# Kernel tuning notes

Hardware: AMD Instinct MI355X
Metric: run time of the kernel (lower is better)

The kernel has to match this reference:

```python
import jax, jax.numpy as jnp
import numpy as np

# Brevitas-style per-tensor affine (symmetric) quantization:
#   scale = max|x| / qmax  (stats-derived, treated as constant)
#   q     = clamp(round(x/scale), qmin, qmax) * scale

def _quant_pt(x, bits):
    qmax = 2.0 ** (bits - 1) - 1.0
    qmin = -(2.0 ** (bits - 1))
    scale = jax.lax.stop_gradient(jnp.max(jnp.abs(x))) / qmax
    scale = jnp.maximum(scale, jnp.asarray(1e-8, x.dtype))
    q = jnp.clip(jnp.round(x / scale), qmin, qmax)
    return q * scale, scale


def setup_inputs() -> dict:
    key = jax.random.key(0)
    k1, k2, k3 = jax.random.split(key, 3)
    in_features, out_features, tokens = 4096, 4096, 8192
    inp = jax.random.normal(k1, (tokens, in_features), dtype=jnp.float32)
    # Kaiming-ish init for linear weight [out, in]
    W = jax.random.normal(k2, (out_features, in_features), dtype=jnp.float32) / np.sqrt(in_features)
    b = jax.random.normal(k3, (out_features,), dtype=jnp.float32) * 0.01
    return {"inp": inp, "W": W, "b": b}


def reference(inp, W, b):
    # input quant: Int8 act per-tensor (QuantIdentity default)
    x_dq, s_in = _quant_pt(inp, 8)
    # weight quant: 4-bit per-tensor
    w_dq, s_w = _quant_pt(W, 4)
    # bias quant: Int32 with scale = s_in * s_w
    s_b = s_in * s_w
    b_dq = jnp.round(b / s_b) * s_b  # int32 range never clips realistic biases
    # matmul in dequantized domain (numerically equal to int GEMM * s_in*s_w)
    y = jnp.einsum('ti,oi->to', x_dq, w_dq) + b_dq
    # output quant: Int8 act per-tensor
    y_dq, _ = _quant_pt(y, 8)
    return y_dq
```

## Files before the change

### kernel.cpp

```cpp
#include <hip/hip_runtime.h>


typedef int v4i __attribute__((ext_vector_type(4)));
typedef int v16i __attribute__((ext_vector_type(16)));

#define AS1(p) ((const __attribute__((address_space(1))) void*)(p))
#define AS3(p) ((__attribute__((address_space(3))) void*)(p))

#define GM 8192
#define GN 4096
#define GK 4096
#define NBN 16
#define NWG 512
#define CH 1088
#define HT 17408

__global__ __launch_bounds__(256) void maxabs2_kernel(const float* __restrict__ x, int n4x,
                                                      unsigned* __restrict__ slotx,
                                                      const float* __restrict__ w, int n4w,
                                                      unsigned* __restrict__ slotw) {
  __shared__ float red[4];
  const float4* src;
  unsigned* slot;
  int n4, bid, nb;
  if (blockIdx.x < 1024) { src = (const float4*)x; slot = slotx; n4 = n4x; bid = blockIdx.x; nb = 1024; }
  else                   { src = (const float4*)w; slot = slotw; n4 = n4w; bid = blockIdx.x - 1024; nb = 512; }
  int tid = bid * 256 + threadIdx.x;
  int stride = nb * 256;
  float m = 0.0f;
  for (int i = tid; i < n4; i += stride) {
    float4 v = src[i];
    m = fmaxf(m, fmaxf(fmaxf(fabsf(v.x), fabsf(v.y)), fmaxf(fabsf(v.z), fabsf(v.w))));
  }
  for (int off = 32; off; off >>= 1) m = fmaxf(m, __shfl_xor(m, off));
  if ((threadIdx.x & 63) == 0) red[threadIdx.x >> 6] = m;
  __syncthreads();
  if (threadIdx.x == 0)
    atomicMax(slot, __float_as_uint(fmaxf(fmaxf(red[0], red[1]), fmaxf(red[2], red[3]))));
}

__global__ __launch_bounds__(256) void quant2_kernel(const float* __restrict__ x,
                                                     signed char* __restrict__ qx, int n4x,
                                                     const unsigned* __restrict__ slotx,
                                                     const float* __restrict__ w,
                                                     signed char* __restrict__ qw, int n4w,
                                                     const unsigned* __restrict__ slotw) {
  const float4* src;
  int* dst;
  int n4, bid, nb;
  float qmaxv, qlo, qhi;
  const unsigned* slot;
  if (blockIdx.x < 1024) {
    src = (const float4*)x; dst = (int*)qx; n4 = n4x; bid = blockIdx.x; nb = 1024;
    slot = slotx; qmaxv = 127.0f; qlo = -128.0f; qhi = 127.0f;
  } else {
    src = (const float4*)w; dst = (int*)qw; n4 = n4w; bid = blockIdx.x - 1024; nb = 512;
    slot = slotw; qmaxv = 7.0f; qlo = -8.0f; qhi = 7.0f;
  }
  float s = fmaxf(__uint_as_float(*slot) / qmaxv, 1e-8f);
  float inv = 1.0f / s;
  int tid = bid * 256 + threadIdx.x;
  int stride = nb * 256;
  for (int i = tid; i < n4; i += stride) {
    float4 v = src[i];
    int a0 = (int)fminf(fmaxf(rintf(v.x * inv), qlo), qhi);
    int a1 = (int)fminf(fmaxf(rintf(v.y * inv), qlo), qhi);
    int a2 = (int)fminf(fmaxf(rintf(v.z * inv), qlo), qhi);
    int a3 = (int)fminf(fmaxf(rintf(v.w * inv), qlo), qhi);
    dst[i] = (a0 & 255) | ((a1 & 255) << 8) | ((a2 & 255) << 16) | ((a3 & 255) << 24);
  }
}

template <bool BF16OUT>
__global__ __launch_bounds__(512, 2) void gemm_i8_kernel(const signed char* __restrict__ Xq,
                                                         const signed char* __restrict__ Wq,
                                                         const float* __restrict__ bias,
                                                         const unsigned* __restrict__ slots,
                                                         void* __restrict__ Yout,
                                                         unsigned* __restrict__ maxY) {
  __shared__ signed char smem[8 * HT];
  const int tid = threadIdx.x;
  const int wid = tid >> 6, lane = tid & 63;
  const int wr = wid >> 2, wc = wid & 3;
  const int l31 = lane & 31, lg2 = lane >> 5;

  const int bid = (int)blockIdx.x;
  const int swz = (bid & 7) * (NWG / 8) + (bid >> 3);
  const int brow = (swz / NBN) * 256;
  const int bcol = (swz % NBN) * 256;

  const int srr = tid >> 3;
  const int sgl = (tid & 7) ^ (srr & 7);

  int aoff[4], asw[4], boff[2], bsw[2];
#pragma unroll
  for (int mm = 0; mm < 4; ++mm) {
    int hr = wr * 64 + (mm & 1) * 32 + l31;
    aoff[mm] = (hr >> 3) * CH + (hr & 7) * 128;
    asw[mm] = hr & 7;
  }
#pragma unroll
  for (int nn = 0; nn < 2; ++nn) {
    int hr = wc * 32 + l31;
    boff[nn] = (hr >> 3) * CH + (hr & 7) * 128;
    bsw[nn] = hr & 7;
  }

#define ASLOT(db, h) (smem + ((db) * 2 + (h)) * HT)
#define BSLOT(db, h) (smem + 4 * HT + ((db) * 2 + (h)) * HT)
#define STAGE(gptr, grow0, kofs, slot)                                                        \
  {                                                                                           \
    const signed char* _s0 = (gptr) + (size_t)((grow0) + srr) * GK + (kofs) + sgl * 16;       \
    __builtin_amdgcn_global_load_lds(AS1(_s0), AS3((slot) + wid * CH), 16, 0, 0);             \
    __builtin_amdgcn_global_load_lds(AS1(_s0 + (size_t)64 * GK),                              \
                                     AS3((slot) + (8 + wid) * CH), 16, 0, 0);                 \
  }
#define LDA32(mm, db, ks) \
  *(const v4i*)(ASLOT(db, (mm) >> 1) + aoff[mm] + ((((ks)*2 + lg2) ^ asw[mm]) << 4))
#define LDB32(nn, db, ks) \
  *(const v4i*)(BSLOT(db, nn) + boff[nn] + ((((ks)*2 + lg2) ^ bsw[nn]) << 4))
#define MFMA8(AF, BF)                                                                         \
  __builtin_amdgcn_s_setprio(1);                                                              \
  _Pragma("unroll") for (int mm = 0; mm < 4; ++mm)                                            \
      _Pragma("unroll") for (int nn = 0; nn < 2; ++nn) acc[mm][nn] =                          \
      __builtin_amdgcn_mfma_i32_32x32x32_i8(AF[mm], BF[nn], acc[mm][nn], 0, 0, 0);            \
  __builtin_amdgcn_s_setprio(0);

  STAGE(Wq, bcol, 0, BSLOT(0, 0));
  STAGE(Wq, bcol + 128, 0, BSLOT(0, 1));
  STAGE(Xq, brow, 0, ASLOT(0, 0));
  STAGE(Xq, brow + 128, 0, ASLOT(0, 1));

  v16i acc[4][2] = {};

#pragma unroll 2
  for (int t = 0; t < 32; ++t) {
    const int db = t & 1, ndb = db ^ 1;
    const int kof = (t + 1) * 128;
    v4i af0[4], af1[4], bf0[2], bf1[2];

    if (t < 31) STAGE(Wq, bcol, kof, BSLOT(ndb, 0));
    if (t == 31)
      asm volatile("s_waitcnt vmcnt(0)" ::: "memory");
    else
      asm volatile("s_waitcnt vmcnt(2)" ::: "memory");
    __builtin_amdgcn_s_barrier();
    asm volatile("" ::: "memory");

#pragma unroll
    for (int mm = 0; mm < 4; ++mm) af0[mm] = LDA32(mm, db, 0);
#pragma unroll
    for (int nn = 0; nn < 2; ++nn) bf0[nn] = LDB32(nn, db, 0);
#pragma unroll
    for (int mm = 0; mm < 4; ++mm) af1[mm] = LDA32(mm, db, 1);
#pragma unroll
    for (int nn = 0; nn < 2; ++nn) bf1[nn] = LDB32(nn, db, 1);
    if (t < 31) STAGE(Wq, bcol + 128, kof, BSLOT(ndb, 1));
    asm volatile("s_waitcnt lgkmcnt(0)");
    MFMA8(af0, bf0)
    MFMA8(af1, bf1)
    __builtin_amdgcn_s_barrier();

#pragma unroll
    for (int mm = 0; mm < 4; ++mm) af0[mm] = LDA32(mm, db, 2);
#pragma unroll
    for (int nn = 0; nn < 2; ++nn) bf0[nn] = LDB32(nn, db, 2);
#pragma unroll
    for (int mm = 0; mm < 4; ++mm) af1[mm] = LDA32(mm, db, 3);
#pragma unroll
    for (int nn = 0; nn < 2; ++nn) bf1[nn] = LDB32(nn, db, 3);
    if (t < 31) {
      STAGE(Xq, brow, kof, ASLOT(ndb, 0));
      STAGE(Xq, brow + 128, kof, ASLOT(ndb, 1));
    }
    asm volatile("s_waitcnt lgkmcnt(0)");
    MFMA8(af0, bf0)
    MFMA8(af1, bf1)
    __builtin_amdgcn_s_barrier();
  }

  float s_in = fmaxf(__uint_as_float(slots[0]) / 127.0f, 1e-8f);
  float s_w = fmaxf(__uint_as_float(slots[1]) / 7.0f, 1e-8f);
  float s_b = s_in * s_w;
  float bdq[2];
#pragma unroll
  for (int nn = 0; nn < 2; ++nn)
    bdq[nn] = rintf(bias[bcol + nn * 128 + wc * 32 + l31] / s_b) * s_b;
  float lmax = 0.0f;
#pragma unroll
  for (int m = 0; m < 4; ++m) {
    int rbase = brow + (m >> 1) * 128 + wr * 64 + (m & 1) * 32 + 4 * lg2;
#pragma unroll
    for (int n = 0; n < 2; ++n) {
      int o = bcol + n * 128 + wc * 32 + l31;
#pragma unroll
      for (int r = 0; r < 16; ++r) {
        int row = rbase + (r & 3) + 8 * (r >> 2);
        float yv = (float)acc[m][n][r] * s_b + bdq[n];
        size_t idx = (size_t)row * GN + o;
        if (BF16OUT) {
          unsigned u = __float_as_uint(yv);
          ((unsigned short*)Yout)[idx] = (unsigned short)((u + 0x7fffu + ((u >> 16) & 1u)) >> 16);
        } else {
          ((float*)Yout)[idx] = yv;
        }
        lmax = fmaxf(lmax, fabsf(yv));
      }
    }
  }
  for (int off = 32; off; off >>= 1) lmax = fmaxf(lmax, __shfl_xor(lmax, off));
  float* fred = (float*)smem;
  if (lane == 0) fred[wid] = lmax;
  __syncthreads();
  if (tid == 0) {
    float m = fred[0];
#pragma unroll
    for (int i = 1; i < 8; ++i) m = fmaxf(m, fred[i]);
    atomicMax(maxY, __float_as_uint(m));
  }
#undef STAGE
#undef ASLOT
#undef BSLOT
#undef LDA32
#undef LDB32
#undef MFMA8
}

__global__ __launch_bounds__(256) void quant_out_bf16_kernel(const unsigned short* __restrict__ yb,
                                                             float* __restrict__ out, int n8,
                                                             const unsigned* __restrict__ slot) {
  float s = fmaxf(__uint_as_float(*slot) / 127.0f, 1e-8f);
  float inv = 1.0f / s;
  int tid = blockIdx.x * blockDim.x + threadIdx.x;
  int stride = gridDim.x * blockDim.x;
  const uint4* y4 = (const uint4*)yb;
  float4* o4 = (float4*)out;
  for (int i = tid; i < n8; i += stride) {
    uint4 v = y4[i];
    float f[8];
    f[0] = __uint_as_float((v.x & 0xffffu) << 16);
    f[1] = __uint_as_float(v.x & 0xffff0000u);
    f[2] = __uint_as_float((v.y & 0xffffu) << 16);
    f[3] = __uint_as_float(v.y & 0xffff0000u);
    f[4] = __uint_as_float((v.z & 0xffffu) << 16);
    f[5] = __uint_as_float(v.z & 0xffff0000u);
    f[6] = __uint_as_float((v.w & 0xffffu) << 16);
    f[7] = __uint_as_float(v.w & 0xffff0000u);
    float4 a, b;
    a.x = fminf(fmaxf(rintf(f[0] * inv), -128.0f), 127.0f) * s;
    a.y = fminf(fmaxf(rintf(f[1] * inv), -128.0f), 127.0f) * s;
    a.z = fminf(fmaxf(rintf(f[2] * inv), -128.0f), 127.0f) * s;
    a.w = fminf(fmaxf(rintf(f[3] * inv), -128.0f), 127.0f) * s;
    b.x = fminf(fmaxf(rintf(f[4] * inv), -128.0f), 127.0f) * s;
    b.y = fminf(fmaxf(rintf(f[5] * inv), -128.0f), 127.0f) * s;
    b.z = fminf(fmaxf(rintf(f[6] * inv), -128.0f), 127.0f) * s;
    b.w = fminf(fmaxf(rintf(f[7] * inv), -128.0f), 127.0f) * s;
    o4[i * 2] = a;
    o4[i * 2 + 1] = b;
  }
}

__global__ __launch_bounds__(256) void quant_out_kernel(float* __restrict__ y, int n4,
                                                        const unsigned* __restrict__ slot) {
  float s = fmaxf(__uint_as_float(*slot) / 127.0f, 1e-8f);
  float inv = 1.0f / s;
  int tid = blockIdx.x * blockDim.x + threadIdx.x;
  int stride = gridDim.x * blockDim.x;
  float4* y4 = (float4*)y;
  for (int i = tid; i < n4; i += stride) {
    float4 v = y4[i];
    v.x = fminf(fmaxf(rintf(v.x * inv), -128.0f), 127.0f) * s;
    v.y = fminf(fmaxf(rintf(v.y * inv), -128.0f), 127.0f) * s;
    v.z = fminf(fmaxf(rintf(v.z * inv), -128.0f), 127.0f) * s;
    v.w = fminf(fmaxf(rintf(v.w * inv), -128.0f), 127.0f) * s;
    y4[i] = v;
  }
}

extern "C" void kernel_launch(void* const* d_in, const int* in_sizes, int n_in,
                              void* d_out, int out_size, void* d_ws, size_t ws_size,
                              hipStream_t stream) {
  const float* inp = (const float*)d_in[0];
  const float* W = (const float*)d_in[1];
  const float* b = (const float*)d_in[2];
  float* out = (float*)d_out;

  unsigned* slots = (unsigned*)d_ws;
  signed char* Xq = (signed char*)d_ws + 256;
  signed char* Wq = Xq + (size_t)GM * GK;
  unsigned short* Yb = (unsigned short*)(Wq + (size_t)GN * GK);

  const int nX = GM * GK;
  const int nW = GN * GK;
  const size_t need_bf16 = 256 + (size_t)nX + (size_t)nW + (size_t)GM * GN * 2;
  const bool use_bf16 = ws_size >= need_bf16;

  hipMemsetAsync(d_ws, 0, 16, stream);

  maxabs2_kernel<<<1536, 256, 0, stream>>>(inp, nX / 4, slots + 0, W, nW / 4, slots + 1);
  quant2_kernel<<<1536, 256, 0, stream>>>(inp, Xq, nX / 4, slots + 0, W, Wq, nW / 4, slots + 1);

  if (use_bf16) {
    gemm_i8_kernel<true><<<NWG, 512, 0, stream>>>(Xq, Wq, b, slots, (void*)Yb, slots + 2);
    quant_out_bf16_kernel<<<1024, 256, 0, stream>>>(Yb, out, (GM * GN) / 8, slots + 2);
  } else {
    gemm_i8_kernel<false><<<NWG, 512, 0, stream>>>(Xq, Wq, b, slots, (void*)out, slots + 2);
    quant_out_kernel<<<1024, 256, 0, stream>>>(out, (GM * GN) / 4, slots + 2);
  }
}
```

Measured before the change: 269.7 us.

## Shrink GEMM tile to 256x128 single-buffered LDS for higher occupancy

The int8 GEMM switches from 256x256 tiles with double-buffered LDS prefetch to 256x128 tiles using a single LDS buffer. Each workgroup loads A and B for one k-step, waits, computes, then moves on. Launch bounds allow four blocks per CU, so latency is hidden by occupancy rather than software pipelining. This trades lower data reuse per tile and lost load/compute overlap within a block for more concurrent workgroups and fewer registers.

Measured after the change: 286.7 us. 1.06x slower.

```diff
diff --git a/kernel.cpp b/kernel.cpp
--- a/kernel.cpp
+++ b/kernel.cpp
@@ -10,8 +10,7 @@
 #define GM 8192
 #define GN 4096
 #define GK 4096
-#define NBN 16
-#define NWG 512
+#define NWG 1024
 #define CH 1088
 #define HT 17408
 
@@ -72,13 +71,13 @@
 }
 
 template <bool BF16OUT>
-__global__ __launch_bounds__(512, 2) void gemm_i8_kernel(const signed char* __restrict__ Xq,
+__global__ __launch_bounds__(512, 4) void gemm_i8_kernel(const signed char* __restrict__ Xq,
                                                          const signed char* __restrict__ Wq,
                                                          const float* __restrict__ bias,
                                                          const unsigned* __restrict__ slots,
                                                          void* __restrict__ Yout,
                                                          unsigned* __restrict__ maxY) {
-  __shared__ signed char smem[8 * HT];
+  __shared__ signed char smem[3 * HT];
   const int tid = threadIdx.x;
   const int wid = tid >> 6, lane = tid & 63;
   const int wr = wid >> 2, wc = wid & 3;
@@ -86,28 +85,27 @@
 
   const int bid = (int)blockIdx.x;
   const int swz = (bid & 7) * (NWG / 8) + (bid >> 3);
-  const int brow = (swz / NBN) * 256;
-  const int bcol = (swz % NBN) * 256;
+  const int brow = (swz >> 5) * 256;
+  const int bcol = (swz & 31) * 128;
 
   const int srr = tid >> 3;
   const int sgl = (tid & 7) ^ (srr & 7);
 
-  int aoff[4], asw[4], boff[2], bsw[2];
+  int aoff[4], asw[4], boffv, bswv;
 #pragma unroll
   for (int mm = 0; mm < 4; ++mm) {
-    int hr = wr * 64 + (mm & 1) * 32 + l31;
+    int hr = mm * 32 + l31;
     aoff[mm] = (hr >> 3) * CH + (hr & 7) * 128;
     asw[mm] = hr & 7;
   }
-#pragma unroll
-  for (int nn = 0; nn < 2; ++nn) {
+  {
     int hr = wc * 32 + l31;
-    boff[nn] = (hr >> 3) * CH + (hr & 7) * 128;
-    bsw[nn] = hr & 7;
-  }
-
-#define ASLOT(db, h) (smem + ((db) * 2 + (h)) * HT)
-#define BSLOT(db, h) (smem + 4 * HT + ((db) * 2 + (h)) * HT)
+    boffv = (hr >> 3) * CH + (hr & 7) * 128;
+    bswv = hr & 7;
+  }
+
+#define ASLOT(h) (smem + (h) * HT)
+#define BSLOT() (smem + 2 * HT)
 #define STAGE(gptr, grow0, kofs, slot)                                                        \
   {                                                                                           \
     const signed char* _s0 = (gptr) + (size_t)((grow0) + srr) * GK + (kofs) + sgl * 16;       \
@@ -115,97 +113,58 @@
     __builtin_amdgcn_global_load_lds(AS1(_s0 + (size_t)64 * GK),                              \
                                      AS3((slot) + (8 + wid) * CH), 16, 0, 0);                 \
   }
-#define LDA32(mm, db, ks) \
-  *(const v4i*)(ASLOT(db, (mm) >> 1) + aoff[mm] + ((((ks)*2 + lg2) ^ asw[mm]) << 4))
-#define LDB32(nn, db, ks) \
-  *(const v4i*)(BSLOT(db, nn) + boff[nn] + ((((ks)*2 + lg2) ^ bsw[nn]) << 4))
-#define MFMA8(AF, BF)                                                                         \
-  __builtin_amdgcn_s_setprio(1);                                                              \
-  _Pragma("unroll") for (int mm = 0; mm < 4; ++mm)                                            \
-      _Pragma("unroll") for (int nn = 0; nn < 2; ++nn) acc[mm][nn] =                          \
-      __builtin_amdgcn_mfma_i32_32x32x32_i8(AF[mm], BF[nn], acc[mm][nn], 0, 0, 0);            \
-  __builtin_amdgcn_s_setprio(0);
-
-  STAGE(Wq, bcol, 0, BSLOT(0, 0));
-  STAGE(Wq, bcol + 128, 0, BSLOT(0, 1));
-  STAGE(Xq, brow, 0, ASLOT(0, 0));
-  STAGE(Xq, brow + 128, 0, ASLOT(0, 1));
-
-  v16i acc[4][2] = {};
-
-#pragma unroll 2
+
+  v16i acc[4] = {};
+
   for (int t = 0; t < 32; ++t) {
-    const int db = t & 1, ndb = db ^ 1;
-    const int kof = (t + 1) * 128;
-    v4i af0[4], af1[4], bf0[2], bf1[2];
-
-    if (t < 31) STAGE(Wq, bcol, kof, BSLOT(ndb, 0));
-    if (t == 31)
-      asm volatile("s_waitcnt vmcnt(0)" ::: "memory");
-    else
-      asm volatile("s_waitcnt vmcnt(2)" ::: "memory");
+    const int kof = t * 128;
+
+    STAGE(Xq, brow, kof, ASLOT(0));
+    STAGE(Xq, brow + 128, kof, ASLOT(1));
+    STAGE(Wq, bcol, kof, BSLOT());
+    asm volatile("s_waitcnt vmcnt(0)" ::: "memory");
     __builtin_amdgcn_s_barrier();
     asm volatile("" ::: "memory");
 
-#pragma unroll
-    for (int mm = 0; mm < 4; ++mm) af0[mm] = LDA32(mm, db, 0);
-#pragma unroll
-    for (int nn = 0; nn < 2; ++nn) bf0[nn] = LDB32(nn, db, 0);
-#pragma unroll
-    for (int mm = 0; mm < 4; ++mm) af1[mm] = LDA32(mm, db, 1);
-#pragma unroll
-    for (int nn = 0; nn < 2; ++nn) bf1[nn] = LDB32(nn, db, 1);
-    if (t < 31) STAGE(Wq, bcol + 128, kof, BSLOT(ndb, 1));
-    asm volatile("s_waitcnt lgkmcnt(0)");
-    MFMA8(af0, bf0)
-    MFMA8(af1, bf1)
+    const signed char* abase = ASLOT(wr);
+#pragma unroll
+    for (int ks = 0; ks < 4; ++ks) {
+      v4i af[4], bf;
+#pragma unroll
+      for (int mm = 0; mm < 4; ++mm)
+        af[mm] = *(const v4i*)(abase + aoff[mm] + (((ks * 2 + lg2) ^ asw[mm]) << 4));
+      bf = *(const v4i*)(BSLOT() + boffv + (((ks * 2 + lg2) ^ bswv) << 4));
+      __builtin_amdgcn_s_setprio(1);
+#pragma unroll
+      for (int mm = 0; mm < 4; ++mm)
+        acc[mm] = __builtin_amdgcn_mfma_i32_32x32x32_i8(af[mm], bf, acc[mm], 0, 0, 0);
+      __builtin_amdgcn_s_setprio(0);
+    }
     __builtin_amdgcn_s_barrier();
-
-#pragma unroll
-    for (int mm = 0; mm < 4; ++mm) af0[mm] = LDA32(mm, db, 2);
-#pragma unroll
-    for (int nn = 0; nn < 2; ++nn) bf0[nn] = LDB32(nn, db, 2);
-#pragma unroll
-    for (int mm = 0; mm < 4; ++mm) af1[mm] = LDA32(mm, db, 3);
-#pragma unroll
-    for (int nn = 0; nn < 2; ++nn) bf1[nn] = LDB32(nn, db, 3);
-    if (t < 31) {
-      STAGE(Xq, brow, kof, ASLOT(ndb, 0));
-      STAGE(Xq, brow + 128, kof, ASLOT(ndb, 1));
-    }
-    asm volatile("s_waitcnt lgkmcnt(0)");
-    MFMA8(af0, bf0)
-    MFMA8(af1, bf1)
-    __builtin_amdgcn_s_barrier();
+    asm volatile("" ::: "memory");
   }
 
   float s_in = fmaxf(__uint_as_float(slots[0]) / 127.0f, 1e-8f);
   float s_w = fmaxf(__uint_as_float(slots[1]) / 7.0f, 1e-8f);
   float s_b = s_in * s_w;
-  float bdq[2];
-#pragma unroll
-  for (int nn = 0; nn < 2; ++nn)
-    bdq[nn] = rintf(bias[bcol + nn * 128 + wc * 32 + l31] / s_b) * s_b;
+  int o = bcol + wc * 32 + l31;
+  float bdq = rintf(bias[o] / s_b) * s_b;
   float lmax = 0.0f;
 #pragma unroll
   for (int m = 0; m < 4; ++m) {
-    int rbase = brow + (m >> 1) * 128 + wr * 64 + (m & 1) * 32 + 4 * lg2;
-#pragma unroll
-    for (int n = 0; n < 2; ++n) {
-      int o = bcol + n * 128 + wc * 32 + l31;
-#pragma unroll
-      for (int r = 0; r < 16; ++r) {
-        int row = rbase + (r & 3) + 8 * (r >> 2);
-        float yv = (float)acc[m][n][r] * s_b + bdq[n];
-        size_t idx = (size_t)row * GN + o;
-        if (BF16OUT) {
-          unsigned u = __float_as_uint(yv);
-          ((unsigned short*)Yout)[idx] = (unsigned short)((u + 0x7fffu + ((u >> 16) & 1u)) >> 16);
-        } else {
-          ((float*)Yout)[idx] = yv;
-        }
-        lmax = fmaxf(lmax, fabsf(yv));
+    int rbase = brow + wr * 128 + m * 32 + 4 * lg2;
+#pragma unroll
+    for (int r = 0; r < 16; ++r) {
+      int row = rbase + (r & 3) + 8 * (r >> 2);
+      float yv = (float)acc[m][r] * s_b + bdq;
+      size_t idx = (size_t)row * GN + o;
+      if (BF16OUT) {
+        unsigned u = __float_as_uint(yv);
+        ((unsigned short*)Yout)[idx] = (unsigned short)((u + 0x7fffu + ((u >> 16) & 1u)) >> 16);
+      } else {
+        ((float*)Yout)[idx] = yv;
       }
+      lmax = fmaxf(lmax, fabsf(yv));
     }
   }
   for (int off = 32; off; off >>= 1) lmax = fmaxf(lmax, __shfl_xor(lmax, off));
@@ -221,9 +180,6 @@
 #undef STAGE
 #undef ASLOT
 #undef BSLOT
-#undef LDA32
-#undef LDB32
-#undef MFMA8
 }
 
 __global__ __launch_bounds__(256) void quant_out_bf16_kernel(const unsigned short* __restrict__ yb,
```
